# Kernel tuning notes

Hardware: AMD Instinct MI355X
Metric: run time of the kernel (lower is better)

The kernel has to match this reference:

```python
import jax, jax.numpy as jnp
import numpy as np
import math

B, T, C = 2, 4096, 768
NH = 12
HS = C // NH

def setup_inputs() -> dict:
    key = jax.random.key(0)
    k1, k2, k3 = jax.random.split(key, 3)
    x = jax.random.normal(k1, (B, T, C), dtype=jnp.float32)
    w_attn = jax.random.normal(k2, (C, 3 * C), dtype=jnp.float32) * (1.0 / math.sqrt(C))
    w_proj = jax.random.normal(k3, (C, C), dtype=jnp.float32) * (1.0 / math.sqrt(C))
    return {"x": x, "w_attn": w_attn, "w_proj": w_proj}

def reference(x, w_attn, w_proj):
    b, t, c = x.shape
    qkv = x @ w_attn                      # [b, t, 3c]
    q, k, v = jnp.split(qkv, 3, axis=-1)
    # [b, nh, t, hs]
    q = q.reshape(b, t, NH, HS).transpose(0, 2, 1, 3)
    k = k.reshape(b, t, NH, HS).transpose(0, 2, 1, 3)
    v = v.reshape(b, t, NH, HS).transpose(0, 2, 1, 3)
    scores = jnp.einsum('bhqd,bhkd->bhqk', q, k) / math.sqrt(HS)
    causal = jnp.tril(jnp.ones((t, t), dtype=bool))
    scores = jnp.where(causal[None, None], scores, -jnp.inf)
    att = jax.nn.softmax(scores, axis=-1)  # dropout p=0 -> identity
    out = jnp.einsum('bhqk,bhkd->bhqd', att, v)
    out = out.transpose(0, 2, 1, 3).reshape(b, t, c)
    return out @ w_proj
```

## Files before the change

### kernel.cpp

```cpp
#include <hip/hip_runtime.h>
#include <hip/hip_bf16.h>
#include <stdint.h>

#define NB 2
#define NT 4096
#define NC 768
#define NHEAD 12
#define HS 64
#define MTOK (NB * NT)
#define C3 (3 * NC)

typedef __bf16 bf16x8 __attribute__((ext_vector_type(8)));
typedef float f32x4 __attribute__((ext_vector_type(4)));
typedef float f32x16 __attribute__((ext_vector_type(16)));

#define KSCALE_LOG2E 0.18033688011f

__device__ __forceinline__ unsigned short f2bf(float f) {
  union { float f; uint32_t u; } v; v.f = f;
  uint32_t r = v.u + 0x7fffu + ((v.u >> 16) & 1u);
  return (unsigned short)(r >> 16);
}
__device__ __forceinline__ unsigned short bft(float f) {
  return (unsigned short)(__builtin_bit_cast(unsigned int, f) >> 16);
}
__device__ __forceinline__ uint32_t pack_bf2(float a, float b) {
  return (__builtin_bit_cast(uint32_t, b) & 0xffff0000u) |
         (__builtin_bit_cast(uint32_t, a) >> 16);
}

__device__ __forceinline__ void gload_lds16(const unsigned short* g, unsigned short* ldsbase) {
  __builtin_amdgcn_global_load_lds(
      (const __attribute__((address_space(1))) unsigned int*)g,
      (__attribute__((address_space(3))) unsigned int*)ldsbase, 16, 0, 0);
}

__device__ __forceinline__ f32x4 mfma16(bf16x8 a, bf16x8 b, f32x4 c) {
  return __builtin_amdgcn_mfma_f32_16x16x32_bf16(a, b, c, 0, 0, 0);
}
__device__ __forceinline__ f32x16 mfma32(bf16x8 a, bf16x8 b, f32x16 c) {
  return __builtin_amdgcn_mfma_f32_32x32x16_bf16(a, b, c, 0, 0, 0);
}

__global__ __launch_bounds__(256) void prep(
    const float* __restrict__ x, const float* __restrict__ wa, const float* __restrict__ wp,
    unsigned short* __restrict__ xb, unsigned short* __restrict__ waT,
    unsigned short* __restrict__ wpT) {
  const int bx = blockIdx.x;
  if (bx < 576) {
    __shared__ float tile[64][65];
    const float* src; unsigned short* dst;
    int srcN, dstN, k0, n0, qscale;
    if (bx < 432) {
      src = wa; dst = waT; srcN = C3; dstN = NC; qscale = 1;
      k0 = (bx / 36) * 64; n0 = (bx % 36) * 64;
    } else {
      const int t = bx - 432;
      src = wp; dst = wpT; srcN = NC; dstN = NC; qscale = 0;
      k0 = (t / 12) * 64; n0 = (t % 12) * 64;
    }
    const int tr = threadIdx.x >> 4;
    const int tc = (threadIdx.x & 15) * 4;
#pragma unroll
    for (int p = 0; p < 4; ++p) {
      const int r = p * 16 + tr;
      const float4 v = *reinterpret_cast<const float4*>(src + (size_t)(k0 + r) * srcN + n0 + tc);
      tile[r][tc + 0] = v.x; tile[r][tc + 1] = v.y;
      tile[r][tc + 2] = v.z; tile[r][tc + 3] = v.w;
    }
    __syncthreads();
#pragma unroll
    for (int p = 0; p < 4; ++p) {
      const int n = p * 16 + tr;
      const float sc = (qscale && (n0 + n) < NC) ? KSCALE_LOG2E : 1.0f;
      ushort4 o;
      o.x = f2bf(tile[tc + 0][n] * sc); o.y = f2bf(tile[tc + 1][n] * sc);
      o.z = f2bf(tile[tc + 2][n] * sc); o.w = f2bf(tile[tc + 3][n] * sc);
      *reinterpret_cast<ushort4*>(dst + (size_t)(n0 + n) * dstN + k0 + tc) = o;
    }
  } else {
    const int gid = (bx - 576) * 256 + threadIdx.x;
    const float4 v = reinterpret_cast<const float4*>(x)[gid];
    ushort4 o;
    o.x = f2bf(v.x); o.y = f2bf(v.y); o.z = f2bf(v.z); o.w = f2bf(v.w);
    reinterpret_cast<ushort4*>(xb)[gid] = o;
  }
}

template <int OUT_BF16>
__global__ __launch_bounds__(256) void gemm128(
    const unsigned short* __restrict__ A,
    const unsigned short* __restrict__ Bt,
    void* __restrict__ Cout,
    unsigned short* __restrict__ vT,
    int M, int N, int K) {
  __shared__ unsigned short smem[2 * 128 * 64];
  unsigned short* As = smem;
  unsigned short* Bs = smem + 128 * 64;

  const int tid = threadIdx.x;
  const int wave = tid >> 6;
  const int lane = tid & 63;
  const int li = lane & 15;
  const int lq = lane >> 4;
  const int wm = wave & 1;
  const int wn = wave >> 1;
  const int row0 = blockIdx.y * 128;
  const int col0 = blockIdx.x * 128;

  const int crow = lane >> 3;
  const int cchunk = ((lane & 7) ^ crow) * 8;

  f32x4 acc[4][4] = {};

  for (int k0 = 0; k0 < K; k0 += 64) {
#pragma unroll
    for (int i = 0; i < 4; ++i) {
      const int R = wave * 32 + i * 8;
      gload_lds16(A + (size_t)(row0 + R + crow) * K + k0 + cchunk, &As[R * 64]);
      gload_lds16(Bt + (size_t)(col0 + R + crow) * K + k0 + cchunk, &Bs[R * 64]);
    }
    __syncthreads();

#pragma unroll
    for (int ks = 0; ks < 2; ++ks) {
      bf16x8 af[4], bf[4];
#pragma unroll
      for (int f = 0; f < 4; ++f) {
        const int arow = wm * 64 + f * 16 + li;
        af[f] = *reinterpret_cast<const bf16x8*>(&As[arow * 64 + (((ks * 4 + lq) ^ (li & 7)) << 3)]);
        const int brow = wn * 64 + f * 16 + li;
        bf[f] = *reinterpret_cast<const bf16x8*>(&Bs[brow * 64 + (((ks * 4 + lq) ^ (li & 7)) << 3)]);
      }
#pragma unroll
      for (int fa = 0; fa < 4; ++fa)
#pragma unroll
        for (int fb = 0; fb < 4; ++fb)
          acc[fa][fb] = mfma16(af[fa], bf[fb], acc[fa][fb]);
    }
    __syncthreads();
  }

  if (OUT_BF16) {
    if (col0 >= 2 * NC) {
      const int b = row0 >> 12;
      const int t0r = row0 & (NT - 1);
      const int h0 = (col0 - 2 * NC) >> 6;
#pragma unroll
      for (int fa = 0; fa < 4; ++fa) {
#pragma unroll
        for (int fb = 0; fb < 4; ++fb) {
          const int cc = wn * 64 + fb * 16 + li;
#pragma unroll
          for (int r = 0; r < 4; ++r) {
            const int tt = wm * 64 + fa * 16 + lq * 4 + r;
            const int slot = cc * 16 + ((tt >> 3) ^ (cc & 15));
            smem[slot * 8 + (tt & 7)] = f2bf(acc[fa][fb][r]);
          }
        }
      }
      __syncthreads();
      const int ch = tid & 15;
#pragma unroll
      for (int j = 0; j < 8; ++j) {
        const int cc = (tid >> 4) + 16 * j;
        const uint4 v = *reinterpret_cast<const uint4*>(
            smem + (size_t)(cc * 16 + (ch ^ (cc & 15))) * 8);
        const int bh = b * NHEAD + h0 + (cc >> 6);
        const int d = cc & 63;
        *reinterpret_cast<uint4*>(vT + (size_t)bh * HS * NT + (size_t)d * NT + t0r + ch * 8) = v;
      }
    } else {
      unsigned short* Cb = (unsigned short*)Cout;
#pragma unroll
      for (int fa = 0; fa < 4; ++fa) {
        const int gr = row0 + wm * 64 + fa * 16 + lq * 4;
#pragma unroll
        for (int fb = 0; fb < 4; ++fb) {
          const int gc = col0 + wn * 64 + fb * 16 + li;
#pragma unroll
          for (int r = 0; r < 4; ++r)
            Cb[(size_t)(gr + r) * N + gc] = f2bf(acc[fa][fb][r]);
        }
      }
    }
  } else {
    float* Cf = (float*)Cout;
#pragma unroll
    for (int fa = 0; fa < 4; ++fa) {
      const int gr = row0 + wm * 64 + fa * 16 + lq * 4;
#pragma unroll
      for (int fb = 0; fb < 4; ++fb) {
        const int gc = col0 + wn * 64 + fb * 16 + li;
#pragma unroll
        for (int r = 0; r < 4; ++r)
          Cf[(size_t)(gr + r) * N + gc] = acc[fa][fb][r];
      }
    }
  }
}


__global__ __launch_bounds__(256) void attn(
    const unsigned short* __restrict__ qkv,
    const unsigned short* __restrict__ vT,
    float* __restrict__ Oacc,
    float* __restrict__ lacc,
    unsigned short* __restrict__ aob) {
  __shared__ unsigned short Ks[3][64 * 64];
  __shared__ unsigned short Vts[3][64 * 64];

  const int tid = threadIdx.x;
  const int wave = tid >> 6;
  const int lane = tid & 63;
  const int l31 = lane & 31;
  const int lh = lane >> 5;
  const int sw = l31 & 7;

  const int bid = (int)blockIdx.x;
  const int w = (bid & 7) * 144 + (bid >> 3);
  const int grp = w / 48;
  const int idx = w - grp * 48;
  const int b = grp / 12;
  const int h = grp - b * 12;
  int qi, tauS, tauE, split;
  if (idx < 32) {
    split = 1;
    qi = 31 - (idx >> 1);
    const int nt = 2 * qi + 2;
    if (idx & 1) { tauS = nt >> 1; tauE = nt; }
    else         { tauS = 0;       tauE = nt >> 1; }
  } else {
    split = 0;
    qi = 47 - idx;
    tauS = 0; tauE = 2 * qi + 2;
  }
  const int q0 = qi * 128;
  const int bh = b * NHEAD + h;

  const size_t baseQ = (size_t)b * NT * C3 + (size_t)h * HS;
  const size_t baseK = baseQ + NC;
  const unsigned short* kq = qkv + baseK;
  const unsigned short* vbase = vT + (size_t)bh * HS * NT;

  const int qw = q0 + wave * 32;
  const int qtok = qw + l31;

  bf16x8 bq[4];
#pragma unroll
  for (int ks = 0; ks < 4; ++ks)
    bq[ks] = *reinterpret_cast<const bf16x8*>(
        qkv + baseQ + (size_t)(qw + l31) * C3 + ks * 16 + lh * 8);

  bf16x8 vones;
#pragma unroll
  for (int i = 0; i < 8; ++i) vones[i] = (__bf16)1.0f;

  f32x16 o0 = {}, o1 = {}, la = {};

  const int grow = lane >> 3;
  const int gch = (lane & 7) ^ grow;
  const int wr0 = wave * 8;
  const int wr1 = wave * 8 + 32;

#define STAGE(TAU, BUFI)                                                        \
  do {                                                                          \
    const int t0s_ = (TAU) * 64;                                                \
    gload_lds16(kq + (size_t)(t0s_ + wr0 + grow) * C3 + gch * 8,                \
                &Ks[BUFI][wr0 * 64]);                                           \
    gload_lds16(kq + (size_t)(t0s_ + wr1 + grow) * C3 + gch * 8,                \
                &Ks[BUFI][wr1 * 64]);                                           \
    gload_lds16(vbase + (size_t)(wr0 + grow) * NT + t0s_ + gch * 8,             \
                &Vts[BUFI][wr0 * 64]);                                          \
    gload_lds16(vbase + (size_t)(wr1 + grow) * NT + t0s_ + gch * 8,             \
                &Vts[BUFI][wr1 * 64]);                                          \
  } while (0)

#define EXP_PACK(ST, KBLK, DOMASK)                                             \
  do {                                                                         \
    const int kb_ = t0 + (KBLK) * 32 + 4 * lh;                                 \
    float p_[16];                                                              \
    _Pragma("unroll") for (int r = 0; r < 16; ++r) {                           \
      float v_ = (ST)[r];                                                      \
      if (DOMASK) {                                                            \
        const int kt_ = kb_ + (r & 3) + 8 * (r >> 2);                          \
        if (kt_ > qtok) v_ = -INFINITY;                                        \
      }                                                                        \
      p_[r] = __builtin_amdgcn_exp2f(v_);                                      \
    }                                                                          \
    _Pragma("unroll") for (int s = 0; s < 2; ++s) {                            \
      uint32_t a_ = pack_bf2(p_[8 * s + 0], p_[8 * s + 1]);                    \
      uint32_t b_ = pack_bf2(p_[8 * s + 2], p_[8 * s + 3]);                    \
      uint32_t c_ = pack_bf2(p_[8 * s + 4], p_[8 * s + 5]);                    \
      uint32_t d_ = pack_bf2(p_[8 * s + 6], p_[8 * s + 7]);                    \
      asm("v_permlane32_swap_b32 %0, %1" : "+v"(a_), "+v"(c_));                \
      asm("v_permlane32_swap_b32 %0, %1" : "+v"(b_), "+v"(d_));                \
      union { uint32_t u[4]; bf16x8 v8; } pu_;                                 \
      pu_.u[0] = a_; pu_.u[1] = b_; pu_.u[2] = c_; pu_.u[3] = d_;              \
      pa[2 * (KBLK) + s] = pu_.v8;                                             \
    }                                                                          \
  } while (0)

#define PV_STEP(KS)                                                            \
  do {                                                                         \
    const int off_ = ((((KS) * 2 + lh) ^ sw) << 3);                            \
    const bf16x8 bv0_ =                                                        \
        *reinterpret_cast<const bf16x8*>(Vc + (size_t)l31 * 64 + off_);        \
    const bf16x8 bv1_ =                                                        \
        *reinterpret_cast<const bf16x8*>(Vc + (size_t)(32 + l31) * 64 + off_); \
    la = mfma32(pa[KS], vones, la);                                            \
    o0 = mfma32(pa[KS], bv0_, o0);                                             \
    o1 = mfma32(pa[KS], bv1_, o1);                                             \
  } while (0)

  STAGE(tauS, 0);
  STAGE(tauS + 1, 1);

  int cur = 0;
  for (int tau = tauS; tau < tauE; ++tau) {
    const int t0 = tau * 64;
    if (tau + 1 < tauE) asm volatile("s_waitcnt vmcnt(4)" ::: "memory");
    else                asm volatile("s_waitcnt vmcnt(0)" ::: "memory");
    __builtin_amdgcn_s_barrier();
    __builtin_amdgcn_sched_barrier(0);
    if (tau + 2 < tauE) {
      int nb = cur + 2; if (nb >= 3) nb -= 3;
      STAGE(tau + 2, nb);
    }

    const unsigned short* Kc = Ks[cur];
    const unsigned short* Vc = Vts[cur];

    if (t0 <= qw + 31) {
      const bool act1 = (t0 + 32 <= qw + 31);
      const bool m0 = (t0 + 31 > qw);
      const bool m1 = (t0 + 63 > qw);

      f32x16 st0 = {}, st1 = {};
      __builtin_amdgcn_s_setprio(1);
#pragma unroll
      for (int ks = 0; ks < 4; ++ks) {
        const bf16x8 ka = *reinterpret_cast<const bf16x8*>(
            Kc + (size_t)l31 * 64 + (((ks * 2 + lh) ^ sw) << 3));
        st0 = mfma32(ka, bq[ks], st0);
      }
      if (act1) {
#pragma unroll
        for (int ks = 0; ks < 4; ++ks) {
          const bf16x8 ka = *reinterpret_cast<const bf16x8*>(
              Kc + (size_t)(32 + l31) * 64 + (((ks * 2 + lh) ^ sw) << 3));
          st1 = mfma32(ka, bq[ks], st1);
        }
      }
      __builtin_amdgcn_s_setprio(0);

      bf16x8 pa[4];
      EXP_PACK(st0, 0, m0);
      if (act1) EXP_PACK(st1, 1, m1);

      __builtin_amdgcn_s_setprio(1);
      PV_STEP(0); PV_STEP(1);
      if (act1) { PV_STEP(2); PV_STEP(3); }
      __builtin_amdgcn_s_setprio(0);
    }
    ++cur; if (cur == 3) cur = 0;
  }
#undef STAGE
#undef EXP_PACK
#undef PV_STEP

  if (split) {
    const size_t obase = (size_t)b * NT * NC + (size_t)h * HS;
    float* lrow = lacc + (size_t)bh * NT;
#pragma unroll
    for (int r = 0; r < 16; ++r) {
      const int q = qw + (r & 3) + 8 * (r >> 2) + 4 * lh;
      if (l31 == 0) atomicAdd(&lrow[q], la[r]);
      atomicAdd(&Oacc[obase + (size_t)q * NC + l31], o0[r]);
      atomicAdd(&Oacc[obase + (size_t)q * NC + 32 + l31], o1[r]);
    }
  } else {
#pragma unroll
    for (int r = 0; r < 16; ++r) {
      const int q = qw + (r & 3) + 8 * (r >> 2) + 4 * lh;
      const float inv = 1.0f / la[r];
      unsigned short* orow = aob + ((size_t)b * NT + q) * NC + h * HS;
      orow[l31] = bft(o0[r] * inv);
      orow[32 + l31] = bft(o1[r] * inv);
    }
  }
}

__global__ __launch_bounds__(256) void finalize(
    const float* __restrict__ Oacc, const float* __restrict__ lacc,
    unsigned short* __restrict__ aob) {
  const int idx4 = (blockIdx.x * 256 + threadIdx.x);
  if (idx4 >= NB * (NT / 2) * NC / 4) return;
  const int idx = idx4 * 4;
  const int rowp = idx / NC;
  const int cc = idx - rowp * NC;
  const int b = rowp >> 11;
  const int t = (NT / 2) + (rowp & 2047);
  const int h = cc >> 6;
  const float inv = 1.0f / lacc[(size_t)(b * NHEAD + h) * NT + t];
  const size_t base = ((size_t)b * NT + t) * NC + cc;
  const float4 v = *reinterpret_cast<const float4*>(Oacc + base);
  ushort4 o;
  o.x = bft(v.x * inv); o.y = bft(v.y * inv);
  o.z = bft(v.z * inv); o.w = bft(v.w * inv);
  *reinterpret_cast<ushort4*>(aob + base) = o;
}

extern "C" void kernel_launch(void* const* d_in, const int* in_sizes, int n_in,
                              void* d_out, int out_size, void* d_ws, size_t ws_size,
                              hipStream_t stream) {
  const float* x = (const float*)d_in[0];
  const float* w_attn = (const float*)d_in[1];
  const float* w_proj = (const float*)d_in[2];
  float* outp = (float*)d_out;

  char* w = (char*)d_ws;
  float* Oacc = (float*)w;
  unsigned short* xb = (unsigned short*)w;
  unsigned short* waT = xb + (size_t)MTOK * NC;
  float* lacc = Oacc + (size_t)MTOK * NC;
  unsigned short* qkvb = (unsigned short*)(lacc + (size_t)NB * NHEAD * NT);
  unsigned short* aob  = qkvb + (size_t)MTOK * C3;
  unsigned short* vTb  = aob + (size_t)MTOK * NC;
  unsigned short* wpT  = vTb + (size_t)MTOK * NC;

  prep<<<576 + MTOK * NC / 4 / 256, 256, 0, stream>>>(x, w_attn, w_proj, xb, waT, wpT);

  gemm128<1><<<dim3(C3 / 128, MTOK / 128), 256, 0, stream>>>(xb, waT, qkvb, vTb, MTOK, C3, NC);

  hipMemsetAsync(Oacc, 0, ((size_t)MTOK * NC + (size_t)NB * NHEAD * NT) * sizeof(float), stream);

  attn<<<1152, 256, 0, stream>>>(qkvb, vTb, Oacc, lacc, aob);

  finalize<<<(NB * (NT / 2) * NC / 4 + 255) / 256, 256, 0, stream>>>(Oacc, lacc, aob);

  gemm128<0><<<dim3(NC / 128, MTOK / 128), 256, 0, stream>>>(aob, wpT, outp, nullptr, MTOK, NC, NC);
}
```

Measured before the change: 259.0 us.

## Use persistent attention blocks with per-XCD atomic work queue and 256-row query tiles

Attention becomes a persistent kernel launched with 768 blocks of 512 threads. Each block pulls work items from a per-XCD atomic counter, following a static, largest-first ordering of query tiles and key splits. Query tiles grow to 256 rows. Tiles beyond the first 512 rows are split into 2 or 4 key ranges that combine via atomics, so finalize now covers rows 512 onward. The aim is better load balance across the causal triangle and more K/V reuse per staged tile, at the cost of extra atomic traffic, the counter overhead and a layout shift in the workspace.

```diff
diff --git a/kernel.cpp b/kernel.cpp
--- a/kernel.cpp
+++ b/kernel.cpp
@@ -201,14 +201,22 @@
 }
 
 
-__global__ __launch_bounds__(256) void attn(
+__device__ const uint8_t g_items[46] = {
+  15,31,47,63, 7,23, 14,30,46,62, 13,29,45,61, 6,22, 12,28,44,60,
+  11,27,43,59, 5,21, 10,26,42,58, 9,25,41,57, 4,20, 8,24,40,56,
+  3,19, 1, 2,18, 0};
+#define ITEMS_PER_XCD (3 * 46)
+
+__global__ __launch_bounds__(512) void attn(
     const unsigned short* __restrict__ qkv,
     const unsigned short* __restrict__ vT,
     float* __restrict__ Oacc,
     float* __restrict__ lacc,
+    unsigned int* __restrict__ ctr,
     unsigned short* __restrict__ aob) {
   __shared__ unsigned short Ks[3][64 * 64];
   __shared__ unsigned short Vts[3][64 * 64];
+  __shared__ unsigned int s_w;
 
   const int tid = threadIdx.x;
   const int wave = tid >> 6;
@@ -216,64 +224,23 @@
   const int l31 = lane & 31;
   const int lh = lane >> 5;
   const int sw = l31 & 7;
-
-  const int bid = (int)blockIdx.x;
-  const int w = (bid & 7) * 144 + (bid >> 3);
-  const int grp = w / 48;
-  const int idx = w - grp * 48;
-  const int b = grp / 12;
-  const int h = grp - b * 12;
-  int qi, tauS, tauE, split;
-  if (idx < 32) {
-    split = 1;
-    qi = 31 - (idx >> 1);
-    const int nt = 2 * qi + 2;
-    if (idx & 1) { tauS = nt >> 1; tauE = nt; }
-    else         { tauS = 0;       tauE = nt >> 1; }
-  } else {
-    split = 0;
-    qi = 47 - idx;
-    tauS = 0; tauE = 2 * qi + 2;
-  }
-  const int q0 = qi * 128;
-  const int bh = b * NHEAD + h;
-
-  const size_t baseQ = (size_t)b * NT * C3 + (size_t)h * HS;
-  const size_t baseK = baseQ + NC;
-  const unsigned short* kq = qkv + baseK;
-  const unsigned short* vbase = vT + (size_t)bh * HS * NT;
-
-  const int qw = q0 + wave * 32;
-  const int qtok = qw + l31;
-
-  bf16x8 bq[4];
-#pragma unroll
-  for (int ks = 0; ks < 4; ++ks)
-    bq[ks] = *reinterpret_cast<const bf16x8*>(
-        qkv + baseQ + (size_t)(qw + l31) * C3 + ks * 16 + lh * 8);
-
-  bf16x8 vones;
-#pragma unroll
-  for (int i = 0; i < 8; ++i) vones[i] = (__bf16)1.0f;
-
-  f32x16 o0 = {}, o1 = {}, la = {};
+  const int xcd = (int)blockIdx.x & 7;
 
   const int grow = lane >> 3;
   const int gch = (lane & 7) ^ grow;
-  const int wr0 = wave * 8;
-  const int wr1 = wave * 8 + 32;
+  const int wr = wave * 8;
+
+  bf16x8 vones;
+#pragma unroll
+  for (int i = 0; i < 8; ++i) vones[i] = (__bf16)1.0f;
 
 #define STAGE(TAU, BUFI)                                                        \
   do {                                                                          \
     const int t0s_ = (TAU) * 64;                                                \
-    gload_lds16(kq + (size_t)(t0s_ + wr0 + grow) * C3 + gch * 8,                \
-                &Ks[BUFI][wr0 * 64]);                                           \
-    gload_lds16(kq + (size_t)(t0s_ + wr1 + grow) * C3 + gch * 8,                \
-                &Ks[BUFI][wr1 * 64]);                                           \
-    gload_lds16(vbase + (size_t)(wr0 + grow) * NT + t0s_ + gch * 8,             \
-                &Vts[BUFI][wr0 * 64]);                                          \
-    gload_lds16(vbase + (size_t)(wr1 + grow) * NT + t0s_ + gch * 8,             \
-                &Vts[BUFI][wr1 * 64]);                                          \
+    gload_lds16(kq + (size_t)(t0s_ + wr + grow) * C3 + gch * 8,                 \
+                &Ks[BUFI][wr * 64]);                                            \
+    gload_lds16(vbase + (size_t)(wr + grow) * NT + t0s_ + gch * 8,              \
+                &Vts[BUFI][wr * 64]);                                           \
   } while (0)
 
 #define EXP_PACK(ST, KBLK, DOMASK)                                             \
@@ -313,94 +280,132 @@
     o1 = mfma32(pa[KS], bv1_, o1);                                             \
   } while (0)
 
-  STAGE(tauS, 0);
-  STAGE(tauS + 1, 1);
-
-  int cur = 0;
-  for (int tau = tauS; tau < tauE; ++tau) {
-    const int t0 = tau * 64;
-    if (tau + 1 < tauE) asm volatile("s_waitcnt vmcnt(4)" ::: "memory");
-    else                asm volatile("s_waitcnt vmcnt(0)" ::: "memory");
-    __builtin_amdgcn_s_barrier();
-    __builtin_amdgcn_sched_barrier(0);
-    if (tau + 2 < tauE) {
-      int nb = cur + 2; if (nb >= 3) nb -= 3;
-      STAGE(tau + 2, nb);
-    }
-
-    const unsigned short* Kc = Ks[cur];
-    const unsigned short* Vc = Vts[cur];
-
-    if (t0 <= qw + 31) {
-      const bool act1 = (t0 + 32 <= qw + 31);
-      const bool m0 = (t0 + 31 > qw);
-      const bool m1 = (t0 + 63 > qw);
-
-      f32x16 st0 = {}, st1 = {};
-      __builtin_amdgcn_s_setprio(1);
-#pragma unroll
-      for (int ks = 0; ks < 4; ++ks) {
-        const bf16x8 ka = *reinterpret_cast<const bf16x8*>(
-            Kc + (size_t)l31 * 64 + (((ks * 2 + lh) ^ sw) << 3));
-        st0 = mfma32(ka, bq[ks], st0);
-      }
-      if (act1) {
+  for (;;) {
+    __syncthreads();
+    if (tid == 0) s_w = atomicAdd(&ctr[xcd], 1u);
+    __syncthreads();
+    const unsigned int w = s_w;
+    if (w >= (unsigned int)ITEMS_PER_XCD) break;
+
+    const int grp = xcd * 3 + (int)(w % 3u);
+    const int e = (int)g_items[w / 3u];
+    const int qj = e & 15;
+    const int part = e >> 4;
+    const int ntile = 4 * qj + 4;
+    int tauS, tauE;
+    if (qj >= 8)      { const int s4 = ntile >> 2; tauS = part * s4; tauE = tauS + s4; }
+    else if (qj >= 2) { const int s2 = ntile >> 1; tauS = part * s2; tauE = tauS + s2; }
+    else              { tauS = 0; tauE = ntile; }
+    const int split = (qj >= 2);
+    const int b = grp / 12;
+    const int h = grp - b * 12;
+    const int bh = grp;
+    const int q0 = qj * 256;
+
+    const size_t baseQ = (size_t)b * NT * C3 + (size_t)h * HS;
+    const unsigned short* kq = qkv + baseQ + NC;
+    const unsigned short* vbase = vT + (size_t)bh * HS * NT;
+
+    const int qw = q0 + wave * 32;
+    const int qtok = qw + l31;
+
+    bf16x8 bq[4];
+#pragma unroll
+    for (int ks = 0; ks < 4; ++ks)
+      bq[ks] = *reinterpret_cast<const bf16x8*>(
+          qkv + baseQ + (size_t)(qw + l31) * C3 + ks * 16 + lh * 8);
+
+    f32x16 o0 = {}, o1 = {}, la = {};
+
+    STAGE(tauS, 0);
+    STAGE(tauS + 1, 1);
+
+    int cur = 0;
+    for (int tau = tauS; tau < tauE; ++tau) {
+      const int t0 = tau * 64;
+      if (tau + 1 < tauE) asm volatile("s_waitcnt vmcnt(2)" ::: "memory");
+      else                asm volatile("s_waitcnt vmcnt(0)" ::: "memory");
+      __builtin_amdgcn_s_barrier();
+      __builtin_amdgcn_sched_barrier(0);
+      if (tau + 2 < tauE) {
+        int nb = cur + 2; if (nb >= 3) nb -= 3;
+        STAGE(tau + 2, nb);
+      }
+
+      const unsigned short* Kc = Ks[cur];
+      const unsigned short* Vc = Vts[cur];
+
+      if (t0 <= qw + 31) {
+        const bool act1 = (t0 + 32 <= qw + 31);
+        const bool m0 = (t0 + 31 > qw);
+        const bool m1 = (t0 + 63 > qw);
+
+        f32x16 st0 = {}, st1 = {};
+        __builtin_amdgcn_s_setprio(1);
 #pragma unroll
         for (int ks = 0; ks < 4; ++ks) {
           const bf16x8 ka = *reinterpret_cast<const bf16x8*>(
-              Kc + (size_t)(32 + l31) * 64 + (((ks * 2 + lh) ^ sw) << 3));
-          st1 = mfma32(ka, bq[ks], st1);
+              Kc + (size_t)l31 * 64 + (((ks * 2 + lh) ^ sw) << 3));
+          st0 = mfma32(ka, bq[ks], st0);
         }
-      }
-      __builtin_amdgcn_s_setprio(0);
-
-      bf16x8 pa[4];
-      EXP_PACK(st0, 0, m0);
-      if (act1) EXP_PACK(st1, 1, m1);
-
-      __builtin_amdgcn_s_setprio(1);
-      PV_STEP(0); PV_STEP(1);
-      if (act1) { PV_STEP(2); PV_STEP(3); }
-      __builtin_amdgcn_s_setprio(0);
-    }
-    ++cur; if (cur == 3) cur = 0;
+        if (act1) {
+#pragma unroll
+          for (int ks = 0; ks < 4; ++ks) {
+            const bf16x8 ka = *reinterpret_cast<const bf16x8*>(
+                Kc + (size_t)(32 + l31) * 64 + (((ks * 2 + lh) ^ sw) << 3));
+            st1 = mfma32(ka, bq[ks], st1);
+          }
+        }
+        __builtin_amdgcn_s_setprio(0);
+
+        bf16x8 pa[4];
+        EXP_PACK(st0, 0, m0);
+        if (act1) EXP_PACK(st1, 1, m1);
+
+        __builtin_amdgcn_s_setprio(1);
+        PV_STEP(0); PV_STEP(1);
+        if (act1) { PV_STEP(2); PV_STEP(3); }
+        __builtin_amdgcn_s_setprio(0);
+      }
+      ++cur; if (cur == 3) cur = 0;
+    }
+
+    if (split) {
+      const size_t obase = (size_t)b * NT * NC + (size_t)h * HS;
+      float* lrow = lacc + (size_t)bh * NT;
+#pragma unroll
+      for (int r = 0; r < 16; ++r) {
+        const int q = qw + (r & 3) + 8 * (r >> 2) + 4 * lh;
+        if (l31 == 0) atomicAdd(&lrow[q], la[r]);
+        atomicAdd(&Oacc[obase + (size_t)q * NC + l31], o0[r]);
+        atomicAdd(&Oacc[obase + (size_t)q * NC + 32 + l31], o1[r]);
+      }
+    } else {
+#pragma unroll
+      for (int r = 0; r < 16; ++r) {
+        const int q = qw + (r & 3) + 8 * (r >> 2) + 4 * lh;
+        const float inv = 1.0f / la[r];
+        unsigned short* orow = aob + ((size_t)b * NT + q) * NC + h * HS;
+        orow[l31] = bft(o0[r] * inv);
+        orow[32 + l31] = bft(o1[r] * inv);
+      }
+    }
   }
 #undef STAGE
 #undef EXP_PACK
 #undef PV_STEP
-
-  if (split) {
-    const size_t obase = (size_t)b * NT * NC + (size_t)h * HS;
-    float* lrow = lacc + (size_t)bh * NT;
-#pragma unroll
-    for (int r = 0; r < 16; ++r) {
-      const int q = qw + (r & 3) + 8 * (r >> 2) + 4 * lh;
-      if (l31 == 0) atomicAdd(&lrow[q], la[r]);
-      atomicAdd(&Oacc[obase + (size_t)q * NC + l31], o0[r]);
-      atomicAdd(&Oacc[obase + (size_t)q * NC + 32 + l31], o1[r]);
-    }
-  } else {
-#pragma unroll
-    for (int r = 0; r < 16; ++r) {
-      const int q = qw + (r & 3) + 8 * (r >> 2) + 4 * lh;
-      const float inv = 1.0f / la[r];
-      unsigned short* orow = aob + ((size_t)b * NT + q) * NC + h * HS;
-      orow[l31] = bft(o0[r] * inv);
-      orow[32 + l31] = bft(o1[r] * inv);
-    }
-  }
 }
 
 __global__ __launch_bounds__(256) void finalize(
     const float* __restrict__ Oacc, const float* __restrict__ lacc,
     unsigned short* __restrict__ aob) {
   const int idx4 = (blockIdx.x * 256 + threadIdx.x);
-  if (idx4 >= NB * (NT / 2) * NC / 4) return;
+  if (idx4 >= NB * (NT - 512) * NC / 4) return;
   const int idx = idx4 * 4;
   const int rowp = idx / NC;
   const int cc = idx - rowp * NC;
-  const int b = rowp >> 11;
-  const int t = (NT / 2) + (rowp & 2047);
+  const int b = (rowp >= (NT - 512)) ? 1 : 0;
+  const int t = 512 + rowp - b * (NT - 512);
   const int h = cc >> 6;
   const float inv = 1.0f / lacc[(size_t)(b * NHEAD + h) * NT + t];
   const size_t base = ((size_t)b * NT + t) * NC + cc;
@@ -424,7 +429,8 @@
   unsigned short* xb = (unsigned short*)w;
   unsigned short* waT = xb + (size_t)MTOK * NC;
   float* lacc = Oacc + (size_t)MTOK * NC;
-  unsigned short* qkvb = (unsigned short*)(lacc + (size_t)NB * NHEAD * NT);
+  unsigned int* ctr = (unsigned int*)(lacc + (size_t)NB * NHEAD * NT);
+  unsigned short* qkvb = (unsigned short*)(ctr + 16);
   unsigned short* aob  = qkvb + (size_t)MTOK * C3;
   unsigned short* vTb  = aob + (size_t)MTOK * NC;
   unsigned short* wpT  = vTb + (size_t)MTOK * NC;
@@ -433,11 +439,13 @@
 
   gemm128<1><<<dim3(C3 / 128, MTOK / 128), 256, 0, stream>>>(xb, waT, qkvb, vTb, MTOK, C3, NC);
 
-  hipMemsetAsync(Oacc, 0, ((size_t)MTOK * NC + (size_t)NB * NHEAD * NT) * sizeof(float), stream);
-
-  attn<<<1152, 256, 0, stream>>>(qkvb, vTb, Oacc, lacc, aob);
-
-  finalize<<<(NB * (NT / 2) * NC / 4 + 255) / 256, 256, 0, stream>>>(Oacc, lacc, aob);
+  hipMemsetAsync(Oacc, 0,
+      ((size_t)MTOK * NC + (size_t)NB * NHEAD * NT) * sizeof(float) + 16 * sizeof(unsigned int),
+      stream);
+
+  attn<<<768, 512, 0, stream>>>(qkvb, vTb, Oacc, lacc, ctr, aob);
+
+  finalize<<<(NB * (NT - 512) * NC / 4 + 255) / 256, 256, 0, stream>>>(Oacc, lacc, aob);
 
   gemm128<0><<<dim3(NC / 128, MTOK / 128), 256, 0, stream>>>(aob, wpT, outp, nullptr, MTOK, NC, NC);
 }
```

Measured after the change: 314.4 us. +21.4%, slower.
